# Optimization experiments

Hardware: AMD Instinct MI355X
Metric: run time of the kernel (lower is better)

The kernel has to match this reference:

```python
import jax, jax.numpy as jnp
import numpy as np

NONLIN = jnp.tanh  # configurable gate/candidate nonlinearity ('nonlin' init arg)

T, B, I, H = 1024, 64, 256, 512


def setup_inputs() -> dict:
    key = jax.random.key(0)
    k1, k2, k3 = jax.random.split(key, 3)
    s_i = 1.0 / np.sqrt(I)
    s_h = 1.0 / np.sqrt(H)
    return {
        "x": jax.random.normal(k1, (T, B, I), dtype=jnp.float32),
        "Wi": jax.random.normal(k2, (I, 4 * H), dtype=jnp.float32) * s_i,
        "Wh": jax.random.normal(k3, (H, 4 * H), dtype=jnp.float32) * s_h,
        "bi": jnp.zeros((4 * H,), dtype=jnp.float32),
        "bh": jnp.zeros((4 * H,), dtype=jnp.float32),
        "h0": jnp.zeros((B, H), dtype=jnp.float32),
        "c0": jnp.zeros((B, H), dtype=jnp.float32),
    }


def reference(x, Wi, Wh, bi, bh, h0, c0):
    # Precompute input projection for all timesteps in one big GEMM: [T,B,4H]
    x_proj = jnp.einsum('tbi,ig->tbg', x, Wi) + bi

    def step(carry, xp_t):
        h, c = carry
        gates = xp_t + h @ Wh + bh            # [B, 4H]
        i_g, f_g, g_g, o_g = jnp.split(gates, 4, axis=-1)
        i_g = jax.nn.sigmoid(i_g)
        f_g = jax.nn.sigmoid(f_g)
        o_g = jax.nn.sigmoid(o_g)
        g_g = NONLIN(g_g)
        c_new = f_g * c + i_g * g_g
        h_new = o_g * NONLIN(c_new)
        return (h_new, c_new), h_new

    (h_T, c_T), hs = jax.lax.scan(step, (h0, c0), x_proj)
    return hs  # [T, B, H] hidden states for every timestep
```

## Files before the change

### kernel.cpp

```cpp
#include <hip/hip_runtime.h>
#include <math.h>


#define TT      1024
#define BB      64
#define II      256
#define HH      512
#define G4H     2048
#define RPB     16
#define NRG     4
#define NCG     64
#define THREADS 512

typedef short  bf16x8 __attribute__((ext_vector_type(8)));
typedef float  f32x4  __attribute__((ext_vector_type(4)));

__device__ __forceinline__ unsigned int cvtpk_bf16(float a, float b) {
    unsigned int r;
    asm volatile("v_cvt_pk_bf16_f32 %0, %1, %2" : "=v"(r) : "v"(a), "v"(b));
    return r;
}
__device__ __forceinline__ void coh_store_u(unsigned int* p, unsigned int v) {
    asm volatile("global_store_dword %0, %1, off sc0 sc1"
                 :: "v"(p), "v"(v) : "memory");
}
__device__ __forceinline__ float fast_tanh(float v) {
    const float e = __expf(-2.0f * fabsf(v));
    const float r = (1.0f - e) / (1.0f + e);
    return v < 0.0f ? -r : r;
}
__device__ __forceinline__ float sigm(float v) {
    return 1.0f / (1.0f + __expf(-v));
}

__device__ __forceinline__ void cvt_frag(float4 v0, float4 v1,
                                         uint4& hi, uint4& lo) {
    hi.x = cvtpk_bf16(v0.x, v0.y);
    hi.y = cvtpk_bf16(v0.z, v0.w);
    hi.z = cvtpk_bf16(v1.x, v1.y);
    hi.w = cvtpk_bf16(v1.z, v1.w);
    lo.x = cvtpk_bf16(v0.x - __uint_as_float(hi.x << 16),
                      v0.y - __uint_as_float(hi.x & 0xffff0000u));
    lo.y = cvtpk_bf16(v0.z - __uint_as_float(hi.y << 16),
                      v0.w - __uint_as_float(hi.y & 0xffff0000u));
    lo.z = cvtpk_bf16(v1.x - __uint_as_float(hi.z << 16),
                      v1.y - __uint_as_float(hi.z & 0xffff0000u));
    lo.w = cvtpk_bf16(v1.z - __uint_as_float(hi.w << 16),
                      v1.w - __uint_as_float(hi.w & 0xffff0000u));
}

__device__ __forceinline__ void unpack8(uint4 a, uint4 b,
                                        uint4& fh, uint4& fl) {
    fh.x = (a.x >> 16) | (a.y & 0xffff0000u);
    fh.y = (a.z >> 16) | (a.w & 0xffff0000u);
    fh.z = (b.x >> 16) | (b.y & 0xffff0000u);
    fh.w = (b.z >> 16) | (b.w & 0xffff0000u);
    fl.x = (a.x & 0xffffu) | (a.y << 16);
    fl.y = (a.z & 0xffffu) | (a.w << 16);
    fl.z = (b.x & 0xffffu) | (b.w == 0 && false ? 0u : (b.w << 16));
    fl.z = (b.x & 0xffffu) | (b.y << 16);
    fl.w = (b.z & 0xffffu) | (b.w << 16);
}

__global__ void init_ctr(unsigned int* c) { c[threadIdx.x] = 0; }

__global__ __launch_bounds__(THREADS) void lstm_persist(
    const float* __restrict__ x,
    const float* __restrict__ Wi,
    const float* __restrict__ Wh,
    const float* __restrict__ bi,
    const float* __restrict__ bh,
    const float* __restrict__ h0p,
    const float* __restrict__ c0p,
    float* __restrict__ out,
    unsigned int* __restrict__ hpk,
    unsigned int* __restrict__ ctr)
{
    const int tid   = threadIdx.x;
    const int cg    = blockIdx.x & 63;
    const int rg    = blockIdx.x >> 6;
    const int row0  = rg * RPB;
    const int cell0 = cg * 8;
    const int wv    = tid >> 6;
    const int lane  = tid & 63;
    const int n2    = wv >> 2;
    const int k4    = wv & 3;

    __shared__ uint4 aFH[24 * 64];
    __shared__ uint4 aFL[24 * 64];
    __shared__ float red[8 * 64 * 4];
    __shared__ float c_lds[RPB][8];

    const int s_ls = tid & 63;
    const int s_r  = s_ls & 15;
    const int s_kb = (tid >> 6) * 32 + ((s_ls >> 4) & 3) * 8;

    bf16x8 wH[6], wL[6];
    {
        const int col = n2 * 16 + (lane & 15);
        const int J   = (col >> 3) * HH + cell0 + (col & 7);
        #pragma unroll
        for (int s = 0; s < 6; ++s) {
            const int kk = (s < 2) ? (k4 * 2 + s) : (8 + k4 * 4 + (s - 2));
            const int kb = kk * 32 + (lane >> 4) * 8;
            float w[8];
            #pragma unroll
            for (int e = 0; e < 8; ++e) {
                const int k = kb + e;
                w[e] = (k < II) ? Wi[(size_t)k * G4H + J]
                                : Wh[(size_t)(k - II) * G4H + J];
            }
            uint4 hi, lo;
            cvt_frag(make_float4(w[0], w[1], w[2], w[3]),
                     make_float4(w[4], w[5], w[6], w[7]), hi, lo);
            wH[s] = *(bf16x8*)&hi;
            wL[s] = *(bf16x8*)&lo;
        }
    }

    float b4[4];
    if (tid < 128) {
        const int r = tid >> 3, m8 = tid & 7;
        #pragma unroll
        for (int g = 0; g < 4; ++g)
            b4[g] = bi[g * HH + cell0 + m8] + bh[g * HH + cell0 + m8];
        c_lds[r][m8] = c0p[(size_t)(row0 + r) * HH + cell0 + m8];
    }

    {
        const float* xr = x + (size_t)(row0 + s_r) * II + s_kb;
        uint4 hi, lo;
        cvt_frag(*(const float4*)xr, *(const float4*)(xr + 4), hi, lo);
        aFH[tid] = hi; aFL[tid] = lo;

        const float* hr = h0p + (size_t)(row0 + s_r) * HH + s_kb;
        cvt_frag(*(const float4*)hr, *(const float4*)(hr + 4), hi, lo);
        aFH[512 + tid] = hi; aFL[512 + tid] = lo;
        cvt_frag(*(const float4*)(hr + 256), *(const float4*)(hr + 260), hi, lo);
        aFH[1024 + tid] = hi; aFL[1024 + tid] = lo;
    }
    __syncthreads();

    f32x4 acc = {0.f, 0.f, 0.f, 0.f};
    #pragma unroll
    for (int q = 0; q < 2; ++q) {
        const int kk = k4 * 2 + q;
        const bf16x8 ah = *(const bf16x8*)&aFH[kk * 64 + lane];
        const bf16x8 al = *(const bf16x8*)&aFL[kk * 64 + lane];
        acc = __builtin_amdgcn_mfma_f32_16x16x32_bf16(ah, wH[q], acc, 0, 0, 0);
        acc = __builtin_amdgcn_mfma_f32_16x16x32_bf16(ah, wL[q], acc, 0, 0, 0);
        acc = __builtin_amdgcn_mfma_f32_16x16x32_bf16(al, wH[q], acc, 0, 0, 0);
    }

    unsigned int* myctr = ctr + rg * 32;

    for (int t = 0; t < TT; ++t) {
        const bool more = (t + 1 < TT);

        float4 xv0, xv1;
        if (more) {
            const float* xr = x + ((size_t)(t + 1) * BB + row0 + s_r) * II + s_kb;
            xv0 = *(const float4*)xr;
            xv1 = *(const float4*)(xr + 4);
        }

        #pragma unroll
        for (int q = 0; q < 4; ++q) {
            const int kk = 8 + k4 * 4 + q;
            const bf16x8 ah = *(const bf16x8*)&aFH[kk * 64 + lane];
            const bf16x8 al = *(const bf16x8*)&aFL[kk * 64 + lane];
            acc = __builtin_amdgcn_mfma_f32_16x16x32_bf16(ah, wH[2 + q], acc, 0, 0, 0);
            acc = __builtin_amdgcn_mfma_f32_16x16x32_bf16(ah, wL[2 + q], acc, 0, 0, 0);
            acc = __builtin_amdgcn_mfma_f32_16x16x32_bf16(al, wH[2 + q], acc, 0, 0, 0);
        }

        ((f32x4*)red)[wv * 64 + lane] = acc;
        if (more) {
            uint4 hi, lo;
            cvt_frag(xv0, xv1, hi, lo);
            aFH[tid] = hi; aFL[tid] = lo;
        }
        __syncthreads();

        if (more && wv >= 2) {
            acc = (f32x4){0.f, 0.f, 0.f, 0.f};
            #pragma unroll
            for (int q = 0; q < 2; ++q) {
                const int kk = k4 * 2 + q;
                const bf16x8 ah = *(const bf16x8*)&aFH[kk * 64 + lane];
                const bf16x8 al = *(const bf16x8*)&aFL[kk * 64 + lane];
                acc = __builtin_amdgcn_mfma_f32_16x16x32_bf16(ah, wH[q], acc, 0, 0, 0);
                acc = __builtin_amdgcn_mfma_f32_16x16x32_bf16(ah, wL[q], acc, 0, 0, 0);
                acc = __builtin_amdgcn_mfma_f32_16x16x32_bf16(al, wH[q], acc, 0, 0, 0);
            }
        }

        if (tid < 128) {
            const int r = tid >> 3, m8 = tid & 7;
            const int lane_c_base = 16 * (r >> 2);
            const int reg = r & 3;
            float g4[4];
            #pragma unroll
            for (int g = 0; g < 4; ++g) {
                const int col = g * 8 + m8;
                const int nn  = col >> 4, cl = col & 15;
                const int lc  = cl + lane_c_base;
                float s = b4[g];
                #pragma unroll
                for (int p = 0; p < 4; ++p)
                    s += red[((nn * 4 + p) * 64 + lc) * 4 + reg];
                g4[g] = s;
            }
            const float ig = sigm(g4[0]);
            const float fg = sigm(g4[1]);
            const float gg = fast_tanh(g4[2]);
            const float og = sigm(g4[3]);
            const float cn = fg * c_lds[r][m8] + ig * gg;
            c_lds[r][m8] = cn;
            const float hv = og * fast_tanh(cn);
            out[((size_t)t * BB + row0 + r) * HH + cell0 + m8] = hv;
            if (more) {
                const unsigned int hb = cvtpk_bf16(hv, hv) & 0xffffu;
                const float hf = __uint_as_float(hb << 16);
                const unsigned int lb = cvtpk_bf16(hv - hf, hv - hf) & 0xffffu;
                coh_store_u(&hpk[((size_t)(t & 1) * BB + row0 + r) * HH
                                 + cell0 + m8], (hb << 16) | lb);
            }
        }

        if (wv < 2) asm volatile("s_waitcnt vmcnt(0) lgkmcnt(0)" ::: "memory");
        __syncthreads();
        if (more) {
            if (tid == 0)
                __hip_atomic_fetch_add(myctr, 1u, __ATOMIC_RELAXED,
                                       __HIP_MEMORY_SCOPE_AGENT);

            if (wv < 2) {
                acc = (f32x4){0.f, 0.f, 0.f, 0.f};
                #pragma unroll
                for (int q = 0; q < 2; ++q) {
                    const int kk = k4 * 2 + q;
                    const bf16x8 ah = *(const bf16x8*)&aFH[kk * 64 + lane];
                    const bf16x8 al = *(const bf16x8*)&aFL[kk * 64 + lane];
                    acc = __builtin_amdgcn_mfma_f32_16x16x32_bf16(ah, wH[q], acc, 0, 0, 0);
                    acc = __builtin_amdgcn_mfma_f32_16x16x32_bf16(ah, wL[q], acc, 0, 0, 0);
                    acc = __builtin_amdgcn_mfma_f32_16x16x32_bf16(al, wH[q], acc, 0, 0, 0);
                }
            }

            if (tid == 0) {
                const unsigned int target = 64u * (unsigned int)(t + 1);
                while (__hip_atomic_load(myctr, __ATOMIC_RELAXED,
                                         __HIP_MEMORY_SCOPE_AGENT) < target) {
                    __builtin_amdgcn_s_sleep(1);
                }
            }
            __syncthreads();

            const unsigned int* hb = hpk + ((size_t)(t & 1) * BB + row0 + s_r) * HH + s_kb;
            uint4 q0, q1, q2, q3;
            asm volatile(
                "global_load_dwordx4 %0, %4, off sc0 sc1\n\t"
                "global_load_dwordx4 %1, %4, off offset:16 sc0 sc1\n\t"
                "global_load_dwordx4 %2, %4, off offset:1024 sc0 sc1\n\t"
                "global_load_dwordx4 %3, %4, off offset:1040 sc0 sc1\n\t"
                "s_waitcnt vmcnt(0)"
                : "=&v"(q0), "=&v"(q1), "=&v"(q2), "=&v"(q3)
                : "v"(hb)
                : "memory");

            {
                uint4 fh, fl;
                unpack8(q0, q1, fh, fl);
                aFH[512 + tid] = fh; aFL[512 + tid] = fl;
                unpack8(q2, q3, fh, fl);
                aFH[1024 + tid] = fh; aFL[1024 + tid] = fl;
            }
            __syncthreads();
        }
    }
}

extern "C" void kernel_launch(void* const* d_in, const int* in_sizes, int n_in,
                              void* d_out, int out_size, void* d_ws, size_t ws_size,
                              hipStream_t stream) {
    const float* x  = (const float*)d_in[0];
    const float* Wi = (const float*)d_in[1];
    const float* Wh = (const float*)d_in[2];
    const float* bi = (const float*)d_in[3];
    const float* bh = (const float*)d_in[4];
    const float* h0 = (const float*)d_in[5];
    const float* c0 = (const float*)d_in[6];
    float* out = (float*)d_out;

    unsigned int* hpk = (unsigned int*)d_ws;
    unsigned int* ctr = (unsigned int*)((char*)d_ws + 2 * BB * HH * 4);

    init_ctr<<<1, 128, 0, stream>>>(ctr);

    void* args[] = { (void*)&x, (void*)&Wi, (void*)&Wh, (void*)&bi,
                     (void*)&bh, (void*)&h0, (void*)&c0, (void*)&out,
                     (void*)&hpk, (void*)&ctr };
    hipError_t e = hipLaunchCooperativeKernel((const void*)lstm_persist,
                                              dim3(NRG * NCG), dim3(THREADS),
                                              args, 0, stream);
    if (e != hipSuccess) {
        (void)hipGetLastError();
        lstm_persist<<<dim3(NRG * NCG), dim3(THREADS), 0, stream>>>(
            x, Wi, Wh, bi, bh, h0, c0, out, hpk, ctr);
    }
}
```

Baseline: 4.294 ms.

## Halve workgroup count by doubling cells per block to 16 with 1024 threads

Reorganizes the persistent LSTM kernel so each workgroup owns 16 hidden cells instead of 8, using 16 waves and 1024 threads. The grid drops from 256 to 128 blocks and each row-group barrier waits on 32 arrivals instead of 64. Each thread now loads one h chunk per step instead of two, and the gate-column mapping simplifies to one gate per wave group. This cuts the cost of the cross-block atomic barrier and spreads the per-step h reload over more threads. In exchange, fewer CUs are busy and each block uses more registers and LDS.

Result: faster. 4.052 ms (-5.6%).

```diff
diff --git a/kernel.cpp b/kernel.cpp
--- a/kernel.cpp
+++ b/kernel.cpp
@@ -9,8 +9,8 @@
 #define G4H     2048
 #define RPB     16
 #define NRG     4
-#define NCG     64
-#define THREADS 512
+#define NCG     32
+#define THREADS 1024
 
 typedef short  bf16x8 __attribute__((ext_vector_type(8)));
 typedef float  f32x4  __attribute__((ext_vector_type(4)));
@@ -57,7 +57,6 @@
     fh.w = (b.z >> 16) | (b.w & 0xffff0000u);
     fl.x = (a.x & 0xffffu) | (a.y << 16);
     fl.y = (a.z & 0xffffu) | (a.w << 16);
-    fl.z = (b.x & 0xffffu) | (b.w == 0 && false ? 0u : (b.w << 16));
     fl.z = (b.x & 0xffffu) | (b.y << 16);
     fl.w = (b.z & 0xffffu) | (b.w << 16);
 }
@@ -77,28 +76,29 @@
     unsigned int* __restrict__ ctr)
 {
     const int tid   = threadIdx.x;
-    const int cg    = blockIdx.x & 63;
-    const int rg    = blockIdx.x >> 6;
+    const int cg    = blockIdx.x & 31;
+    const int rg    = blockIdx.x >> 5;
     const int row0  = rg * RPB;
-    const int cell0 = cg * 8;
+    const int cell0 = cg * 16;
     const int wv    = tid >> 6;
     const int lane  = tid & 63;
-    const int n2    = wv >> 2;
+    const int n4    = wv >> 2;
     const int k4    = wv & 3;
 
     __shared__ uint4 aFH[24 * 64];
     __shared__ uint4 aFL[24 * 64];
-    __shared__ float red[8 * 64 * 4];
-    __shared__ float c_lds[RPB][8];
+    __shared__ float red[16 * 64 * 4];
+    __shared__ float c_lds[RPB][16];
 
     const int s_ls = tid & 63;
     const int s_r  = s_ls & 15;
-    const int s_kb = (tid >> 6) * 32 + ((s_ls >> 4) & 3) * 8;
+    const int s_k2 = ((s_ls >> 4) & 3) * 8;
+    const int xkk  = tid >> 6;
+    const int hkc  = (tid >> 6) * 32 + s_k2;
 
     bf16x8 wH[6], wL[6];
     {
-        const int col = n2 * 16 + (lane & 15);
-        const int J   = (col >> 3) * HH + cell0 + (col & 7);
+        const int J = n4 * HH + cell0 + (lane & 15);
         #pragma unroll
         for (int s = 0; s < 6; ++s) {
             const int kk = (s < 2) ? (k4 * 2 + s) : (8 + k4 * 4 + (s - 2));
@@ -119,25 +119,25 @@
     }
 
     float b4[4];
-    if (tid < 128) {
-        const int r = tid >> 3, m8 = tid & 7;
+    if (tid < 256) {
+        const int r = tid >> 4, m = tid & 15;
         #pragma unroll
         for (int g = 0; g < 4; ++g)
-            b4[g] = bi[g * HH + cell0 + m8] + bh[g * HH + cell0 + m8];
-        c_lds[r][m8] = c0p[(size_t)(row0 + r) * HH + cell0 + m8];
-    }
-
-    {
-        const float* xr = x + (size_t)(row0 + s_r) * II + s_kb;
+            b4[g] = bi[g * HH + cell0 + m] + bh[g * HH + cell0 + m];
+        c_lds[r][m] = c0p[(size_t)(row0 + r) * HH + cell0 + m];
+    }
+
+    if (tid < 512) {
+        const float* xr = x + (size_t)(row0 + s_r) * II + xkk * 32 + s_k2;
         uint4 hi, lo;
         cvt_frag(*(const float4*)xr, *(const float4*)(xr + 4), hi, lo);
         aFH[tid] = hi; aFL[tid] = lo;
-
-        const float* hr = h0p + (size_t)(row0 + s_r) * HH + s_kb;
+    }
+    {
+        const float* hr = h0p + (size_t)(row0 + s_r) * HH + hkc;
+        uint4 hi, lo;
         cvt_frag(*(const float4*)hr, *(const float4*)(hr + 4), hi, lo);
         aFH[512 + tid] = hi; aFL[512 + tid] = lo;
-        cvt_frag(*(const float4*)(hr + 256), *(const float4*)(hr + 260), hi, lo);
-        aFH[1024 + tid] = hi; aFL[1024 + tid] = lo;
     }
     __syncthreads();
 
@@ -158,8 +158,9 @@
         const bool more = (t + 1 < TT);
 
         float4 xv0, xv1;
-        if (more) {
-            const float* xr = x + ((size_t)(t + 1) * BB + row0 + s_r) * II + s_kb;
+        if (more && tid < 512) {
+            const float* xr = x + ((size_t)(t + 1) * BB + row0 + s_r) * II
+                              + xkk * 32 + s_k2;
             xv0 = *(const float4*)xr;
             xv1 = *(const float4*)(xr + 4);
         }
@@ -175,14 +176,14 @@
         }
 
         ((f32x4*)red)[wv * 64 + lane] = acc;
-        if (more) {
+        if (more && tid < 512) {
             uint4 hi, lo;
             cvt_frag(xv0, xv1, hi, lo);
             aFH[tid] = hi; aFL[tid] = lo;
         }
         __syncthreads();
 
-        if (more && wv >= 2) {
+        if (more && wv >= 4) {
             acc = (f32x4){0.f, 0.f, 0.f, 0.f};
             #pragma unroll
             for (int q = 0; q < 2; ++q) {
@@ -195,47 +196,44 @@
             }
         }
 
-        if (tid < 128) {
-            const int r = tid >> 3, m8 = tid & 7;
-            const int lane_c_base = 16 * (r >> 2);
+        if (tid < 256) {
+            const int r = tid >> 4, m = tid & 15;
+            const int lc  = m + 16 * (r >> 2);
             const int reg = r & 3;
             float g4[4];
             #pragma unroll
             for (int g = 0; g < 4; ++g) {
-                const int col = g * 8 + m8;
-                const int nn  = col >> 4, cl = col & 15;
-                const int lc  = cl + lane_c_base;
                 float s = b4[g];
                 #pragma unroll
                 for (int p = 0; p < 4; ++p)
-                    s += red[((nn * 4 + p) * 64 + lc) * 4 + reg];
+                    s += red[((g * 4 + p) * 64 + lc) * 4 + reg];
                 g4[g] = s;
             }
             const float ig = sigm(g4[0]);
             const float fg = sigm(g4[1]);
             const float gg = fast_tanh(g4[2]);
             const float og = sigm(g4[3]);
-            const float cn = fg * c_lds[r][m8] + ig * gg;
-            c_lds[r][m8] = cn;
+            const float cn = fg * c_lds[r][m] + ig * gg;
+            c_lds[r][m] = cn;
             const float hv = og * fast_tanh(cn);
-            out[((size_t)t * BB + row0 + r) * HH + cell0 + m8] = hv;
+            out[((size_t)t * BB + row0 + r) * HH + cell0 + m] = hv;
             if (more) {
                 const unsigned int hb = cvtpk_bf16(hv, hv) & 0xffffu;
                 const float hf = __uint_as_float(hb << 16);
                 const unsigned int lb = cvtpk_bf16(hv - hf, hv - hf) & 0xffffu;
                 coh_store_u(&hpk[((size_t)(t & 1) * BB + row0 + r) * HH
-                                 + cell0 + m8], (hb << 16) | lb);
-            }
-        }
-
-        if (wv < 2) asm volatile("s_waitcnt vmcnt(0) lgkmcnt(0)" ::: "memory");
+                                 + cell0 + m], (hb << 16) | lb);
+            }
+        }
+
+        if (wv < 4) asm volatile("s_waitcnt vmcnt(0) lgkmcnt(0)" ::: "memory");
         __syncthreads();
         if (more) {
             if (tid == 0)
                 __hip_atomic_fetch_add(myctr, 1u, __ATOMIC_RELAXED,
                                        __HIP_MEMORY_SCOPE_AGENT);
 
-            if (wv < 2) {
+            if (wv < 4) {
                 acc = (f32x4){0.f, 0.f, 0.f, 0.f};
                 #pragma unroll
                 for (int q = 0; q < 2; ++q) {
@@ -249,7 +247,7 @@
             }
 
             if (tid == 0) {
-                const unsigned int target = 64u * (unsigned int)(t + 1);
+                const unsigned int target = 32u * (unsigned int)(t + 1);
                 while (__hip_atomic_load(myctr, __ATOMIC_RELAXED,
                                          __HIP_MEMORY_SCOPE_AGENT) < target) {
                     __builtin_amdgcn_s_sleep(1);
@@ -257,15 +255,13 @@
             }
             __syncthreads();
 
-            const unsigned int* hb = hpk + ((size_t)(t & 1) * BB + row0 + s_r) * HH + s_kb;
-            uint4 q0, q1, q2, q3;
+            const unsigned int* hb = hpk + ((size_t)(t & 1) * BB + row0 + s_r) * HH + hkc;
+            uint4 q0, q1;
             asm volatile(
-                "global_load_dwordx4 %0, %4, off sc0 sc1\n\t"
-                "global_load_dwordx4 %1, %4, off offset:16 sc0 sc1\n\t"
-                "global_load_dwordx4 %2, %4, off offset:1024 sc0 sc1\n\t"
-                "global_load_dwordx4 %3, %4, off offset:1040 sc0 sc1\n\t"
+                "global_load_dwordx4 %0, %2, off sc0 sc1\n\t"
+                "global_load_dwordx4 %1, %2, off offset:16 sc0 sc1\n\t"
                 "s_waitcnt vmcnt(0)"
-                : "=&v"(q0), "=&v"(q1), "=&v"(q2), "=&v"(q3)
+                : "=&v"(q0), "=&v"(q1)
                 : "v"(hb)
                 : "memory");
 
@@ -273,8 +269,6 @@
                 uint4 fh, fl;
                 unpack8(q0, q1, fh, fl);
                 aFH[512 + tid] = fh; aFL[512 + tid] = fl;
-                unpack8(q2, q3, fh, fl);
-                aFH[1024 + tid] = fh; aFL[1024 + tid] = fl;
             }
             __syncthreads();
         }
```
